# Kernel tuning notes

Measured on AMD Instinct MI355X. Metric: run time of the kernel, lower is better.

The kernel has to match this reference:

```python
import jax, jax.numpy as jnp
import numpy as np

IN_F = 8192
OUT_F = 8192
M = 32  # tokens (small -> memory-bound dequant+GEMV-like)


def setup_inputs() -> dict:
    key = jax.random.key(0)
    k1, k2, k3 = jax.random.split(key, 3)
    x = jax.random.normal(k1, (M, IN_F), dtype=jnp.float32)
    # int8-range quantized weights, stored as int8 like the torch buffer
    weight_quantized = jax.random.randint(k2, (OUT_F, IN_F), -128, 128, dtype=jnp.int32).astype(jnp.int8)
    # positive per-output-channel scales (clamped min 1e-8 in quantize())
    weight_scale = jax.random.uniform(k3, (OUT_F,), dtype=jnp.float32) * 0.02 + 1e-8
    return {"x": x, "weight_quantized": weight_quantized, "weight_scale": weight_scale}


def reference(x, weight_quantized, weight_scale):
    # dequantize: W[o,i] = int8[o,i] * scale[o]  (full fp32 materialization, as in source)
    w = weight_quantized.astype(jnp.float32) * weight_scale[:, None]  # [OUT_F, IN_F]
    # F.linear: x @ W^T
    return jnp.einsum('mi,oi->mo', x, w)
```

## Files before the change

kernel.cpp:

```cpp
#include <hip/hip_runtime.h>
#include <stdint.h>

#define IN_F   8192
#define OUT_F  8192
#define M_TOK  32
#define BN     32
#define BK     128
#define NIT    (IN_F / BK)
#define PF     2
#define LDSS   136

typedef float  f32x4  __attribute__((ext_vector_type(4)));
typedef short  short8 __attribute__((ext_vector_type(8)));

#define LDS_BARRIER() do {                                   \
    asm volatile("s_waitcnt lgkmcnt(0)" ::: "memory");       \
    __builtin_amdgcn_s_barrier();                            \
} while (0)

__device__ inline unsigned pk_bf16(float f0, float f1) {
    unsigned u0 = __builtin_bit_cast(unsigned, f0);
    unsigned u1 = __builtin_bit_cast(unsigned, f1);
    return (u0 >> 16) | (u1 & 0xFFFF0000u);
}

__global__ __launch_bounds__(256) void qlin_mfma(
    const float* __restrict__ x, const int* __restrict__ wq,
    const float* __restrict__ scale, float* __restrict__ out) {

    __shared__ ushort ldsA[2][M_TOK][LDSS];
    __shared__ ushort ldsW[2][BN][LDSS];

    const int t  = threadIdx.x;
    const int o0 = blockIdx.x * BN;

    const int r  = t >> 3;
    const int cc = (t & 7) * 16;

    const float* xp = x  + (size_t)r * IN_F + cc;
    const int*   wp = wq + (size_t)(o0 + r) * IN_F + cc;

    float4 abuf[PF][4];
    int4   wbuf[PF][4];

    #pragma unroll
    for (int p = 0; p < PF; ++p) {
        #pragma unroll
        for (int q = 0; q < 4; ++q) {
            abuf[p][q] = *reinterpret_cast<const float4*>(xp + p * BK + 4 * q);
            wbuf[p][q] = *reinterpret_cast<const int4*>(wp + p * BK + 4 * q);
        }
    }

    const int wid  = t >> 6;
    const int lane = t & 63;
    const int mt   = wid & 1;
    const int nt   = wid >> 1;
    const int frow = lane & 15;
    const int fk   = (lane >> 4) * 8;

    f32x4 acc = {0.f, 0.f, 0.f, 0.f};

    for (int base = 0; base < NIT; base += PF) {
        #pragma unroll
        for (int p = 0; p < PF; ++p) {
            const int it  = base + p;
            const int buf = it & 1;

            {
                float4 v0 = abuf[p][0], v1 = abuf[p][1];
                float4 v2 = abuf[p][2], v3 = abuf[p][3];
                uint4 w0, w1;
                w0.x = pk_bf16(v0.x, v0.y); w0.y = pk_bf16(v0.z, v0.w);
                w0.z = pk_bf16(v1.x, v1.y); w0.w = pk_bf16(v1.z, v1.w);
                w1.x = pk_bf16(v2.x, v2.y); w1.y = pk_bf16(v2.z, v2.w);
                w1.z = pk_bf16(v3.x, v3.y); w1.w = pk_bf16(v3.z, v3.w);
                *reinterpret_cast<uint4*>(&ldsA[buf][r][cc])     = w0;
                *reinterpret_cast<uint4*>(&ldsA[buf][r][cc + 8]) = w1;
            }
            {
                int4 a0 = wbuf[p][0], a1 = wbuf[p][1];
                int4 a2 = wbuf[p][2], a3 = wbuf[p][3];
                uint4 w0, w1;
                w0.x = pk_bf16((float)a0.x, (float)a0.y);
                w0.y = pk_bf16((float)a0.z, (float)a0.w);
                w0.z = pk_bf16((float)a1.x, (float)a1.y);
                w0.w = pk_bf16((float)a1.z, (float)a1.w);
                w1.x = pk_bf16((float)a2.x, (float)a2.y);
                w1.y = pk_bf16((float)a2.z, (float)a2.w);
                w1.z = pk_bf16((float)a3.x, (float)a3.y);
                w1.w = pk_bf16((float)a3.z, (float)a3.w);
                *reinterpret_cast<uint4*>(&ldsW[buf][r][cc])     = w0;
                *reinterpret_cast<uint4*>(&ldsW[buf][r][cc + 8]) = w1;
            }

            const int nit = it + PF;
            if (nit < NIT) {
                #pragma unroll
                for (int q = 0; q < 4; ++q) {
                    abuf[p][q] = *reinterpret_cast<const float4*>(xp + nit * BK + 4 * q);
                    wbuf[p][q] = *reinterpret_cast<const int4*>(wp + nit * BK + 4 * q);
                }
            }

            LDS_BARRIER();

            const ushort* aB = &ldsA[buf][mt * 16 + frow][fk];
            const ushort* wB = &ldsW[buf][nt * 16 + frow][fk];
            #pragma unroll
            for (int ks = 0; ks < 4; ++ks) {
                short8 af = *reinterpret_cast<const short8*>(aB + ks * 32);
                short8 bf = *reinterpret_cast<const short8*>(wB + ks * 32);
                acc = __builtin_amdgcn_mfma_f32_16x16x32_bf16(af, bf, acc, 0, 0, 0);
            }
        }
    }

    const int ocol = o0 + nt * 16 + frow;
    const float s  = scale[ocol];
    const int  m0  = mt * 16 + (lane >> 4) * 4;
    #pragma unroll
    for (int rg = 0; rg < 4; ++rg)
        out[(size_t)(m0 + rg) * OUT_F + ocol] = acc[rg] * s;
}

extern "C" void kernel_launch(void* const* d_in, const int* in_sizes, int n_in,
                              void* d_out, int out_size, void* d_ws, size_t ws_size,
                              hipStream_t stream) {
    const float* x  = (const float*)d_in[0];
    const int*   wq = (const int*)d_in[1];
    const float* sc = (const float*)d_in[2];
    float* out = (float*)d_out;

    qlin_mfma<<<OUT_F / BN, 256, 0, stream>>>(x, wq, sc, out);
}
```

Baseline: 53.59 us.

## Halve output tile per block and split K across waves with LDS reduction

Each block now covers 16 output channels instead of 32, which doubles the grid to 512 blocks so more CUs get work. The four waves are split into two M tiles by two K halves, and the K halves are summed through a small LDS buffer at the end. Launch bounds now request two blocks per CU. The cost is that each block re-reads and re-converts the full x activation tile for only 16 outputs, doubling total x traffic and conversion work.

```diff
diff --git a/kernel.cpp b/kernel.cpp
--- a/kernel.cpp
+++ b/kernel.cpp
@@ -4,7 +4,7 @@
 #define IN_F   8192
 #define OUT_F  8192
 #define M_TOK  32
-#define BN     32
+#define BN     16
 #define BK     128
 #define NIT    (IN_F / BK)
 #define PF     2
@@ -24,38 +24,41 @@
     return (u0 >> 16) | (u1 & 0xFFFF0000u);
 }
 
-__global__ __launch_bounds__(256) void qlin_mfma(
+__global__ __launch_bounds__(256, 2) void qlin_mfma(
     const float* __restrict__ x, const int* __restrict__ wq,
     const float* __restrict__ scale, float* __restrict__ out) {
 
     __shared__ ushort ldsA[2][M_TOK][LDSS];
     __shared__ ushort ldsW[2][BN][LDSS];
+    __shared__ f32x4  red[2][64];
 
     const int t  = threadIdx.x;
     const int o0 = blockIdx.x * BN;
 
-    const int r  = t >> 3;
-    const int cc = (t & 7) * 16;
+    const int ra  = t >> 3;
+    const int ca  = (t & 7) * 16;
+    const int rw  = t >> 4;
+    const int cw  = (t & 15) * 8;
 
-    const float* xp = x  + (size_t)r * IN_F + cc;
-    const int*   wp = wq + (size_t)(o0 + r) * IN_F + cc;
+    const float* xp = x  + (size_t)ra * IN_F + ca;
+    const int*   wp = wq + (size_t)(o0 + rw) * IN_F + cw;
 
     float4 abuf[PF][4];
-    int4   wbuf[PF][4];
+    int4   wbuf[PF][2];
 
     #pragma unroll
     for (int p = 0; p < PF; ++p) {
         #pragma unroll
-        for (int q = 0; q < 4; ++q) {
+        for (int q = 0; q < 4; ++q)
             abuf[p][q] = *reinterpret_cast<const float4*>(xp + p * BK + 4 * q);
-            wbuf[p][q] = *reinterpret_cast<const int4*>(wp + p * BK + 4 * q);
-        }
+        wbuf[p][0] = *reinterpret_cast<const int4*>(wp + p * BK);
+        wbuf[p][1] = *reinterpret_cast<const int4*>(wp + p * BK + 4);
     }
 
     const int wid  = t >> 6;
     const int lane = t & 63;
     const int mt   = wid & 1;
-    const int nt   = wid >> 1;
+    const int kh   = wid >> 1;
     const int frow = lane & 15;
     const int fk   = (lane >> 4) * 8;
 
@@ -75,40 +78,34 @@
                 w0.z = pk_bf16(v1.x, v1.y); w0.w = pk_bf16(v1.z, v1.w);
                 w1.x = pk_bf16(v2.x, v2.y); w1.y = pk_bf16(v2.z, v2.w);
                 w1.z = pk_bf16(v3.x, v3.y); w1.w = pk_bf16(v3.z, v3.w);
-                *reinterpret_cast<uint4*>(&ldsA[buf][r][cc])     = w0;
-                *reinterpret_cast<uint4*>(&ldsA[buf][r][cc + 8]) = w1;
+                *reinterpret_cast<uint4*>(&ldsA[buf][ra][ca])     = w0;
+                *reinterpret_cast<uint4*>(&ldsA[buf][ra][ca + 8]) = w1;
             }
             {
                 int4 a0 = wbuf[p][0], a1 = wbuf[p][1];
-                int4 a2 = wbuf[p][2], a3 = wbuf[p][3];
-                uint4 w0, w1;
+                uint4 w0;
                 w0.x = pk_bf16((float)a0.x, (float)a0.y);
                 w0.y = pk_bf16((float)a0.z, (float)a0.w);
                 w0.z = pk_bf16((float)a1.x, (float)a1.y);
                 w0.w = pk_bf16((float)a1.z, (float)a1.w);
-                w1.x = pk_bf16((float)a2.x, (float)a2.y);
-                w1.y = pk_bf16((float)a2.z, (float)a2.w);
-                w1.z = pk_bf16((float)a3.x, (float)a3.y);
-                w1.w = pk_bf16((float)a3.z, (float)a3.w);
-                *reinterpret_cast<uint4*>(&ldsW[buf][r][cc])     = w0;
-                *reinterpret_cast<uint4*>(&ldsW[buf][r][cc + 8]) = w1;
+                *reinterpret_cast<uint4*>(&ldsW[buf][rw][cw]) = w0;
             }
 
             const int nit = it + PF;
             if (nit < NIT) {
                 #pragma unroll
-                for (int q = 0; q < 4; ++q) {
+                for (int q = 0; q < 4; ++q)
                     abuf[p][q] = *reinterpret_cast<const float4*>(xp + nit * BK + 4 * q);
-                    wbuf[p][q] = *reinterpret_cast<const int4*>(wp + nit * BK + 4 * q);
-                }
+                wbuf[p][0] = *reinterpret_cast<const int4*>(wp + nit * BK);
+                wbuf[p][1] = *reinterpret_cast<const int4*>(wp + nit * BK + 4);
             }
 
             LDS_BARRIER();
 
-            const ushort* aB = &ldsA[buf][mt * 16 + frow][fk];
-            const ushort* wB = &ldsW[buf][nt * 16 + frow][fk];
+            const ushort* aB = &ldsA[buf][mt * 16 + frow][kh * 64 + fk];
+            const ushort* wB = &ldsW[buf][frow][kh * 64 + fk];
             #pragma unroll
-            for (int ks = 0; ks < 4; ++ks) {
+            for (int ks = 0; ks < 2; ++ks) {
                 short8 af = *reinterpret_cast<const short8*>(aB + ks * 32);
                 short8 bf = *reinterpret_cast<const short8*>(wB + ks * 32);
                 acc = __builtin_amdgcn_mfma_f32_16x16x32_bf16(af, bf, acc, 0, 0, 0);
@@ -116,12 +113,17 @@
         }
     }
 
-    const int ocol = o0 + nt * 16 + frow;
-    const float s  = scale[ocol];
-    const int  m0  = mt * 16 + (lane >> 4) * 4;
-    #pragma unroll
-    for (int rg = 0; rg < 4; ++rg)
-        out[(size_t)(m0 + rg) * OUT_F + ocol] = acc[rg] * s;
+    if (kh == 1) red[mt][lane] = acc;
+    __syncthreads();
+    if (kh == 0) {
+        f32x4 s = acc + red[mt][lane];
+        const int   ocol = o0 + frow;
+        const float sc   = scale[ocol];
+        const int   m0   = mt * 16 + (lane >> 4) * 4;
+        #pragma unroll
+        for (int rg = 0; rg < 4; ++rg)
+            out[(size_t)(m0 + rg) * OUT_F + ocol] = s[rg] * sc;
+    }
 }
 
 extern "C" void kernel_launch(void* const* d_in, const int* in_sizes, int n_in,
```

New measurement: 63.56 us. +18.6%, slower.

## Split K dimension across two blocks with a separate reduction kernel

Applied to the files above, without the earlier changes.

Splits the 8192-long reduction into two halves, so the grid grows from 256 to 512 blocks. Each block writes its partial 32x32 tile to workspace, and a second kernel sums the two partials and applies the per-channel scale. The aim is to fill more of the GPU's compute units and keep more memory traffic in flight during the weight stream. The cost is a second kernel launch and an extra workspace write and read.

```diff
diff --git a/kernel.cpp b/kernel.cpp
--- a/kernel.cpp
+++ b/kernel.cpp
@@ -5,8 +5,10 @@
 #define OUT_F  8192
 #define M_TOK  32
 #define BN     32
+#define KSPLIT 2
+#define KLEN   (IN_F / KSPLIT)
 #define BK     128
-#define NIT    (IN_F / BK)
+#define NIT    (KLEN / BK)
 #define PF     2
 #define LDSS   136
 
@@ -24,21 +26,23 @@
     return (u0 >> 16) | (u1 & 0xFFFF0000u);
 }
 
-__global__ __launch_bounds__(256) void qlin_mfma(
+__global__ __launch_bounds__(256, 2) void qlin_part(
     const float* __restrict__ x, const int* __restrict__ wq,
-    const float* __restrict__ scale, float* __restrict__ out) {
+    float* __restrict__ wsp) {
 
     __shared__ ushort ldsA[2][M_TOK][LDSS];
     __shared__ ushort ldsW[2][BN][LDSS];
 
     const int t  = threadIdx.x;
-    const int o0 = blockIdx.x * BN;
+    const int b  = blockIdx.x >> 1;
+    const int kb = blockIdx.x & 1;
+    const int o0 = b * BN;
 
     const int r  = t >> 3;
     const int cc = (t & 7) * 16;
 
-    const float* xp = x  + (size_t)r * IN_F + cc;
-    const int*   wp = wq + (size_t)(o0 + r) * IN_F + cc;
+    const float* xp = x  + (size_t)r * IN_F + (size_t)kb * KLEN + cc;
+    const int*   wp = wq + (size_t)(o0 + r) * IN_F + (size_t)kb * KLEN + cc;
 
     float4 abuf[PF][4];
     int4   wbuf[PF][4];
@@ -116,12 +120,33 @@
         }
     }
 
-    const int ocol = o0 + nt * 16 + frow;
-    const float s  = scale[ocol];
-    const int  m0  = mt * 16 + (lane >> 4) * 4;
+    float* wsb = wsp + (size_t)blockIdx.x * (32 * 32);
+    const int ocl = nt * 16 + frow;
+    const int m0  = mt * 16 + (lane >> 4) * 4;
     #pragma unroll
     for (int rg = 0; rg < 4; ++rg)
-        out[(size_t)(m0 + rg) * OUT_F + ocol] = acc[rg] * s;
+        wsb[(m0 + rg) * 32 + ocl] = acc[rg];
+}
+
+__global__ __launch_bounds__(256) void qred(
+    const float* __restrict__ wsp, const float* __restrict__ scale,
+    float* __restrict__ out) {
+    const int b  = blockIdx.x;
+    const int t  = threadIdx.x;
+    const int m  = t >> 3;
+    const int c0 = (t & 7) * 4;
+
+    const float* p0 = wsp + (size_t)(2 * b) * 1024;
+    const float* p1 = p0 + 1024;
+    float4 a = *reinterpret_cast<const float4*>(p0 + m * 32 + c0);
+    float4 c = *reinterpret_cast<const float4*>(p1 + m * 32 + c0);
+    float4 s = *reinterpret_cast<const float4*>(scale + b * 32 + c0);
+    float4 rv;
+    rv.x = (a.x + c.x) * s.x;
+    rv.y = (a.y + c.y) * s.y;
+    rv.z = (a.z + c.z) * s.z;
+    rv.w = (a.w + c.w) * s.w;
+    *reinterpret_cast<float4*>(out + (size_t)m * OUT_F + b * 32 + c0) = rv;
 }
 
 extern "C" void kernel_launch(void* const* d_in, const int* in_sizes, int n_in,
@@ -131,6 +156,8 @@
     const int*   wq = (const int*)d_in[1];
     const float* sc = (const float*)d_in[2];
     float* out = (float*)d_out;
+    float* wsp = (float*)d_ws;
 
-    qlin_mfma<<<OUT_F / BN, 256, 0, stream>>>(x, wq, sc, out);
+    qlin_part<<<OUT_F / BN * KSPLIT, 256, 0, stream>>>(x, wq, wsp);
+    qred<<<OUT_F / BN, 256, 0, stream>>>(wsp, sc, out);
 }
```

Measured after the change: 59.29 us. +10.6%, slower.
